# Kernel tuning notes

Measured on AMD Instinct MI355X. Metric: run time of the kernel, lower is better.

## Reference

```python
import jax, jax.numpy as jnp
import numpy as np

K_NEIGH = 5          # topk(..., k=5) hardcoded in compute_distance
CLIP = 1.0 - 1e-7    # keep arccos/grad finite under fp roundoff of unit-quat dots


def setup_inputs() -> dict:
    key = jax.random.key(0)
    k1, k2 = jax.random.split(key)
    pose = jax.random.normal(k1, (1024, 21, 4), dtype=jnp.float32)
    tp = jax.random.normal(k2, (10000, 21, 4), dtype=jnp.float32)
    # train_poses are unit quaternions per joint (module assumes pre-normalized bank)
    train_poses = tp / jnp.linalg.norm(tp, axis=-1, keepdims=True)
    return {"pose": pose, "train_poses": train_poses}


def reference(pose, train_poses):
    # F.normalize(pose, dim=2): unit quaternion per joint
    rand = pose / jnp.linalg.norm(pose, axis=-1, keepdims=True)
    # per-joint quaternion dot: [N, M, 21] (avoids the repeat() materialization of the original)
    dots = jnp.einsum('njd,mjd->nmj', rand, train_poses)
    dots = jnp.clip(dots, -CLIP, CLIP)
    # geodesic distance: sum_j arccos(dot_j) / 2  -> [N, M]
    dist = jnp.sum(jnp.arccos(dots), axis=2) * 0.5
    # smallest-5 neighbors along M, then mean -> [N]
    neg_top, _ = jax.lax.top_k(-dist, K_NEIGH)
    dist_vals = jnp.mean(-neg_top, axis=1)
    return dist_vals
```

## Files before the change

### kernel.cpp

```cpp
#include <hip/hip_runtime.h>
#include <math.h>

#define N_POSE   1024
#define M_TRAIN  10000
#define NJOINT   21
#define KNEIGH   5
#define CLIPV    (1.0f - 1e-7f)
#define PI_F     3.14159265358979f
#define HPI_F    1.57079632679490f
#define BIGF     1e30f
#define QN_FLOATS (N_POSE * NJOINT * 4)

__global__ __launch_bounds__(256)
void pose_norm_kernel(const float* __restrict__ pose, float* __restrict__ qn) {
    int i = blockIdx.x * blockDim.x + threadIdx.x;
    if (i >= N_POSE * NJOINT) return;
    float4 v = ((const float4*)pose)[i];
    float inv = rsqrtf(v.x * v.x + v.y * v.y + v.z * v.z + v.w * v.w);
    v.x *= inv; v.y *= inv; v.z *= inv; v.w *= inv;
    ((float4*)qn)[i] = v;
}

__global__ __launch_bounds__(64)
void pose_dist_kernel(const float* __restrict__ qn,
                      const float* __restrict__ train,
                      float* __restrict__ topk,
                      int chunks, int mchunk) {
    const int nb = blockIdx.x / chunks;
    const int cb = blockIdx.x % chunks;
    const int n  = nb * 64 + threadIdx.x;

    float4 q[NJOINT];
    const float4* __restrict__ qp = (const float4*)qn + (size_t)n * NJOINT;
#pragma unroll
    for (int j = 0; j < NJOINT; ++j) q[j] = qp[j];
#pragma unroll
    for (int j = 0; j < NJOINT; ++j)
        asm volatile("" : "+v"(q[j].x), "+v"(q[j].y), "+v"(q[j].z), "+v"(q[j].w));

    float t0 = BIGF, t1 = BIGF, t2 = BIGF, t3 = BIGF, t4 = BIGF;
    const float4* __restrict__ tq = (const float4*)train + (size_t)cb * mchunk * NJOINT;

#pragma unroll 1
    for (int mi = 0; mi < mchunk; ++mi) {
        const float4* __restrict__ tm = tq + (size_t)mi * NJOINT;
        float a0 = 0.f, a1 = 0.f;
#pragma unroll
        for (int j = 0; j < NJOINT; ++j) {
            float4 p = q[j];
            float4 u = tm[j];
            float d = u.x * p.x + u.y * p.y + u.z * p.z + u.w * p.w;
            float a = fminf(fabsf(d), CLIPV);
            float pl = fmaf(a, -0.0187293f, 0.0742610f);
            pl = fmaf(a, pl, -0.2121144f);
            pl = fmaf(a, pl, 1.5707288f);
            float r  = __builtin_amdgcn_sqrtf(1.0f - a) * pl;
            float cs = __builtin_copysignf(HPI_F - r, d);
            if (j & 1) a1 += cs; else a0 += cs;
        }
        float v = (NJOINT * HPI_F - (a0 + a1)) * 0.5f;
        t4 = fminf(t4, fmaxf(t3, v));
        t3 = fminf(t3, fmaxf(t2, v));
        t2 = fminf(t2, fmaxf(t1, v));
        t1 = fminf(t1, fmaxf(t0, v));
        t0 = fminf(t0, v);
    }

    float* w = topk + ((size_t)n * chunks + cb) * KNEIGH;
    w[0] = t0; w[1] = t1; w[2] = t2; w[3] = t3; w[4] = t4;
}

__global__ __launch_bounds__(64)
void pose_reduce_kernel(const float* __restrict__ topk, float* __restrict__ out,
                        int chunks) {
    const int n = blockIdx.x;
    const int lane = threadIdx.x;
    const int total = chunks * KNEIGH;
    const float* __restrict__ w = topk + (size_t)n * total;

    float t0 = BIGF, t1 = BIGF, t2 = BIGF, t3 = BIGF, t4 = BIGF;
    for (int i = lane; i < total; i += 64) {
        float v = w[i];
        t4 = fminf(t4, fmaxf(t3, v));
        t3 = fminf(t3, fmaxf(t2, v));
        t2 = fminf(t2, fmaxf(t1, v));
        t1 = fminf(t1, fmaxf(t0, v));
        t0 = fminf(t0, v);
    }

    float sum = 0.f;
#pragma unroll
    for (int r = 0; r < KNEIGH; ++r) {
        float v = t0; int who = lane;
        for (int off = 32; off; off >>= 1) {
            float ov = __shfl_xor(v, off);
            int   ow = __shfl_xor(who, off);
            if (ov < v || (ov == v && ow < who)) { v = ov; who = ow; }
        }
        sum += v;
        if (lane == who) { t0 = t1; t1 = t2; t2 = t3; t3 = t4; t4 = BIGF; }
    }
    if (lane == 0) out[n] = sum * (1.0f / KNEIGH);
}

extern "C" void kernel_launch(void* const* d_in, const int* in_sizes, int n_in,
                              void* d_out, int out_size, void* d_ws, size_t ws_size,
                              hipStream_t stream) {
    const float* pose  = (const float*)d_in[0];
    const float* train = (const float*)d_in[1];
    float* out  = (float*)d_out;
    float* qn   = (float*)d_ws;
    float* topk = (float*)d_ws + QN_FLOATS;

    size_t base = (size_t)QN_FLOATS * sizeof(float);
    int chunks = 250;
    if (base + (size_t)N_POSE * chunks * KNEIGH * sizeof(float) > ws_size) chunks = 125;
    if (base + (size_t)N_POSE * chunks * KNEIGH * sizeof(float) > ws_size) chunks = 50;
    if (base + (size_t)N_POSE * chunks * KNEIGH * sizeof(float) > ws_size) chunks = 10;
    const int mchunk = M_TRAIN / chunks;

    pose_norm_kernel<<<dim3((N_POSE * NJOINT + 255) / 256), dim3(256), 0, stream>>>(pose, qn);

    dim3 grid1((N_POSE / 64) * chunks);
    pose_dist_kernel<<<grid1, dim3(64), 0, stream>>>(qn, train, topk, chunks, mchunk);

    pose_reduce_kernel<<<dim3(N_POSE), dim3(64), 0, stream>>>(topk, out, chunks);
}
```

Baseline: 107.0 us.

## Split joints across wave halves and combine partial distances with a cross-lane shuffle

Each 64-lane block now covers 32 poses. The two half-waves each handle about half of the 21 joints: 11 for one half, 10 plus a padded zeroed slot for the other. Partial arccos sums are combined with a shuffle across lane 32 before the top-5 update. This halves per-thread register use for query quaternions and doubles the number of blocks, aiming at better occupancy and latency hiding. In exchange it spends one wasted joint slot and a cross-lane shuffle per train sample, and duplicates the top-5 maintenance in both halves.

Result: slower. 155.0 us (+44.9%).

```diff
diff --git a/kernel.cpp b/kernel.cpp
--- a/kernel.cpp
+++ b/kernel.cpp
@@ -6,9 +6,9 @@
 #define NJOINT   21
 #define KNEIGH   5
 #define CLIPV    (1.0f - 1e-7f)
-#define PI_F     3.14159265358979f
 #define HPI_F    1.57079632679490f
 #define BIGF     1e30f
+#define JH       11
 #define QN_FLOATS (N_POSE * NJOINT * 4)
 
 __global__ __launch_bounds__(256)
@@ -26,29 +26,37 @@
                       const float* __restrict__ train,
                       float* __restrict__ topk,
                       int chunks, int mchunk) {
-    const int nb = blockIdx.x / chunks;
-    const int cb = blockIdx.x % chunks;
-    const int n  = nb * 64 + threadIdx.x;
+    const int nb   = blockIdx.x / chunks;
+    const int cb   = blockIdx.x % chunks;
+    const int lane = threadIdx.x;
+    const int h    = lane >> 5;
+    const int n    = nb * 32 + (lane & 31);
+    const int jbase = h * JH;
 
-    float4 q[NJOINT];
-    const float4* __restrict__ qp = (const float4*)qn + (size_t)n * NJOINT;
+    float4 q[JH];
+    const float4* __restrict__ qp = (const float4*)qn + (size_t)n * NJOINT + jbase;
 #pragma unroll
-    for (int j = 0; j < NJOINT; ++j) q[j] = qp[j];
+    for (int jj = 0; jj < JH; ++jj) {
+        int o = jj; if (jbase + jj > NJOINT - 1) o = jj - 1;
+        q[jj] = qp[o];
+    }
 #pragma unroll
-    for (int j = 0; j < NJOINT; ++j)
-        asm volatile("" : "+v"(q[j].x), "+v"(q[j].y), "+v"(q[j].z), "+v"(q[j].w));
+    for (int jj = 0; jj < JH; ++jj)
+        asm volatile("" : "+v"(q[jj].x), "+v"(q[jj].y), "+v"(q[jj].z), "+v"(q[jj].w));
 
     float t0 = BIGF, t1 = BIGF, t2 = BIGF, t3 = BIGF, t4 = BIGF;
-    const float4* __restrict__ tq = (const float4*)train + (size_t)cb * mchunk * NJOINT;
+    const float4* __restrict__ tq =
+        (const float4*)train + (size_t)cb * mchunk * NJOINT + jbase;
 
 #pragma unroll 1
     for (int mi = 0; mi < mchunk; ++mi) {
         const float4* __restrict__ tm = tq + (size_t)mi * NJOINT;
         float a0 = 0.f, a1 = 0.f;
 #pragma unroll
-        for (int j = 0; j < NJOINT; ++j) {
-            float4 p = q[j];
-            float4 u = tm[j];
+        for (int jj = 0; jj < JH; ++jj) {
+            int o = jj; if (jbase + jj > NJOINT - 1) o = jj - 1;
+            float4 p = q[jj];
+            float4 u = tm[o];
             float d = u.x * p.x + u.y * p.y + u.z * p.z + u.w * p.w;
             float a = fminf(fabsf(d), CLIPV);
             float pl = fmaf(a, -0.0187293f, 0.0742610f);
@@ -56,9 +64,11 @@
             pl = fmaf(a, pl, 1.5707288f);
             float r  = __builtin_amdgcn_sqrtf(1.0f - a) * pl;
             float cs = __builtin_copysignf(HPI_F - r, d);
-            if (j & 1) a1 += cs; else a0 += cs;
+            if (jj == JH - 1) cs = h ? 0.f : cs;
+            if (jj & 1) a1 += cs; else a0 += cs;
         }
-        float v = (NJOINT * HPI_F - (a0 + a1)) * 0.5f;
+        float acc = a0 + a1;
+        float v = (NJOINT * HPI_F - (acc + __shfl_xor(acc, 32))) * 0.5f;
         t4 = fminf(t4, fmaxf(t3, v));
         t3 = fminf(t3, fmaxf(t2, v));
         t2 = fminf(t2, fmaxf(t1, v));
@@ -66,8 +76,10 @@
         t0 = fminf(t0, v);
     }
 
-    float* w = topk + ((size_t)n * chunks + cb) * KNEIGH;
-    w[0] = t0; w[1] = t1; w[2] = t2; w[3] = t3; w[4] = t4;
+    if (lane < 32) {
+        float* w = topk + ((size_t)n * chunks + cb) * KNEIGH;
+        w[0] = t0; w[1] = t1; w[2] = t2; w[3] = t3; w[4] = t4;
+    }
 }
 
 __global__ __launch_bounds__(64)
@@ -121,7 +133,7 @@
 
     pose_norm_kernel<<<dim3((N_POSE * NJOINT + 255) / 256), dim3(256), 0, stream>>>(pose, qn);
 
-    dim3 grid1((N_POSE / 64) * chunks);
+    dim3 grid1((N_POSE / 32) * chunks);
     pose_dist_kernel<<<grid1, dim3(64), 0, stream>>>(qn, train, topk, chunks, mchunk);
 
     pose_reduce_kernel<<<dim3(N_POSE), dim3(64), 0, stream>>>(topk, out, chunks);
```

## Split joints across four lanes per pose and reduce partial sums via shuffles

Applied to the files above, without the earlier changes.

Each pose is now handled by four lanes that each take 5 or 6 joints, so a 256-thread block covers 64 poses with four times as many threads and far fewer registers per thread. Partial arccos sums are combined with two xor shuffles. The top-5 is tracked as a max over the sum, with the final distance transform moved into the reduce kernel, and a branch skips the insertion when the value cannot enter the top-5. The cost is redundant top-k work on all lanes, extra shuffles, a masked duplicate joint load for three of the four lane groups, and inline asm loads.

New measurement: 145.6 us. +36.1%, slower.

```diff
diff --git a/kernel.cpp b/kernel.cpp
--- a/kernel.cpp
+++ b/kernel.cpp
@@ -6,10 +6,18 @@
 #define NJOINT   21
 #define KNEIGH   5
 #define CLIPV    (1.0f - 1e-7f)
-#define PI_F     3.14159265358979f
 #define HPI_F    1.57079632679490f
 #define BIGF     1e30f
+#define TPB      256
 #define QN_FLOATS (N_POSE * NJOINT * 4)
+
+typedef float v4f __attribute__((ext_vector_type(4)));
+
+__device__ __forceinline__ v4f qload(const float* a) {
+    v4f r;
+    asm volatile("global_load_dwordx4 %0, %1, off" : "=v"(r) : "v"(a) : "memory");
+    return r;
+}
 
 __global__ __launch_bounds__(256)
 void pose_norm_kernel(const float* __restrict__ pose, float* __restrict__ qn) {
@@ -21,34 +29,41 @@
     ((float4*)qn)[i] = v;
 }
 
-__global__ __launch_bounds__(64)
+__global__ __launch_bounds__(TPB)
 void pose_dist_kernel(const float* __restrict__ qn,
                       const float* __restrict__ train,
                       float* __restrict__ topk,
                       int chunks, int mchunk) {
-    const int nb = blockIdx.x / chunks;
-    const int cb = blockIdx.x % chunks;
-    const int n  = nb * 64 + threadIdx.x;
+    const int nb  = blockIdx.x / chunks;
+    const int cb  = blockIdx.x % chunks;
+    const int tid = threadIdx.x;
+    const int wl  = tid & 63;
+    const int h   = wl >> 4;
+    const int n   = nb * 64 + (tid >> 6) * 16 + (wl & 15);
+    const int jbase = (h == 0) ? 0 : (5 * h + 1);
+    const int cnt   = (h == 0) ? 6 : 5;
+    const int off5  = (cnt - 1) * 4;
+    const float mask5 = (h == 0) ? 1.0f : 0.0f;
 
-    float4 q[NJOINT];
-    const float4* __restrict__ qp = (const float4*)qn + (size_t)n * NJOINT;
+    v4f q[6];
+    const float* qb = qn + (size_t)n * (NJOINT * 4) + jbase * 4;
 #pragma unroll
-    for (int j = 0; j < NJOINT; ++j) q[j] = qp[j];
-#pragma unroll
-    for (int j = 0; j < NJOINT; ++j)
-        asm volatile("" : "+v"(q[j].x), "+v"(q[j].y), "+v"(q[j].z), "+v"(q[j].w));
+    for (int jj = 0; jj < 5; ++jj) q[jj] = qload(qb + jj * 4);
+    q[5] = qload(qb + off5);
+    asm volatile("s_waitcnt vmcnt(0)" ::: "memory");
 
-    float t0 = BIGF, t1 = BIGF, t2 = BIGF, t3 = BIGF, t4 = BIGF;
-    const float4* __restrict__ tq = (const float4*)train + (size_t)cb * mchunk * NJOINT;
+    float t0 = -BIGF, t1 = -BIGF, t2 = -BIGF, t3 = -BIGF, t4 = -BIGF;
+    const float* tb = train + (size_t)cb * mchunk * (NJOINT * 4) + jbase * 4;
 
 #pragma unroll 1
     for (int mi = 0; mi < mchunk; ++mi) {
-        const float4* __restrict__ tm = tq + (size_t)mi * NJOINT;
+        const float* tm = tb + (size_t)mi * (NJOINT * 4);
         float a0 = 0.f, a1 = 0.f;
 #pragma unroll
-        for (int j = 0; j < NJOINT; ++j) {
-            float4 p = q[j];
-            float4 u = tm[j];
+        for (int jj = 0; jj < 6; ++jj) {
+            float4 u = (jj < 5) ? ((const float4*)tm)[jj]
+                                : *(const float4*)(tm + off5);
+            v4f p = q[jj];
             float d = u.x * p.x + u.y * p.y + u.z * p.z + u.w * p.w;
             float a = fminf(fabsf(d), CLIPV);
             float pl = fmaf(a, -0.0187293f, 0.0742610f);
@@ -56,18 +71,25 @@
             pl = fmaf(a, pl, 1.5707288f);
             float r  = __builtin_amdgcn_sqrtf(1.0f - a) * pl;
             float cs = __builtin_copysignf(HPI_F - r, d);
-            if (j & 1) a1 += cs; else a0 += cs;
+            if (jj == 5) cs *= mask5;
+            if (jj & 1) a1 += cs; else a0 += cs;
         }
-        float v = (NJOINT * HPI_F - (a0 + a1)) * 0.5f;
-        t4 = fminf(t4, fmaxf(t3, v));
-        t3 = fminf(t3, fmaxf(t2, v));
-        t2 = fminf(t2, fmaxf(t1, v));
-        t1 = fminf(t1, fmaxf(t0, v));
-        t0 = fminf(t0, v);
+        float S = a0 + a1;
+        S += __shfl_xor(S, 16);
+        S += __shfl_xor(S, 32);
+        if (S > t4) {
+            t4 = fmaxf(t4, fminf(t3, S));
+            t3 = fmaxf(t3, fminf(t2, S));
+            t2 = fmaxf(t2, fminf(t1, S));
+            t1 = fmaxf(t1, fminf(t0, S));
+            t0 = fmaxf(t0, S);
+        }
     }
 
-    float* w = topk + ((size_t)n * chunks + cb) * KNEIGH;
-    w[0] = t0; w[1] = t1; w[2] = t2; w[3] = t3; w[4] = t4;
+    if (wl < 16) {
+        float* w = topk + ((size_t)n * chunks + cb) * KNEIGH;
+        w[0] = t0; w[1] = t1; w[2] = t2; w[3] = t3; w[4] = t4;
+    }
 }
 
 __global__ __launch_bounds__(64)
@@ -80,7 +102,7 @@
 
     float t0 = BIGF, t1 = BIGF, t2 = BIGF, t3 = BIGF, t4 = BIGF;
     for (int i = lane; i < total; i += 64) {
-        float v = w[i];
+        float v = (NJOINT * HPI_F - w[i]) * 0.5f;
         t4 = fminf(t4, fmaxf(t3, v));
         t3 = fminf(t3, fmaxf(t2, v));
         t2 = fminf(t2, fmaxf(t1, v));
@@ -122,7 +144,7 @@
     pose_norm_kernel<<<dim3((N_POSE * NJOINT + 255) / 256), dim3(256), 0, stream>>>(pose, qn);
 
     dim3 grid1((N_POSE / 64) * chunks);
-    pose_dist_kernel<<<grid1, dim3(64), 0, stream>>>(qn, train, topk, chunks, mchunk);
+    pose_dist_kernel<<<grid1, dim3(TPB), 0, stream>>>(qn, train, topk, chunks, mchunk);
 
     pose_reduce_kernel<<<dim3(N_POSE), dim3(64), 0, stream>>>(topk, out, chunks);
 }
```

## Stream transposed query joints and process eight train poses per joint

Applied to the files above, without the earlier changes.

The normalization kernel now writes query quaternions in a joint-major transposed layout. The distance kernel streams one joint at a time from that layout instead of holding all 21 quaternions in registers. Each loop step evaluates 8 train poses per joint with independent accumulators, and blocks grow from 64 to 256 threads. The aim is to cut VGPR pressure and raise ILP and occupancy, at the cost of re-reading query data from cache on every 8-pose block.

Result: slower. 113.1 us (+5.8%).

```diff
diff --git a/kernel.cpp b/kernel.cpp
--- a/kernel.cpp
+++ b/kernel.cpp
@@ -6,64 +6,75 @@
 #define NJOINT   21
 #define KNEIGH   5
 #define CLIPV    (1.0f - 1e-7f)
-#define PI_F     3.14159265358979f
 #define HPI_F    1.57079632679490f
 #define BIGF     1e30f
-#define QN_FLOATS (N_POSE * NJOINT * 4)
+#define TPB      256
+#define MB       8
+#define QT_FLOATS (N_POSE * NJOINT * 4)
 
 __global__ __launch_bounds__(256)
-void pose_norm_kernel(const float* __restrict__ pose, float* __restrict__ qn) {
+void pose_norm_t_kernel(const float* __restrict__ pose, float* __restrict__ qT) {
     int i = blockIdx.x * blockDim.x + threadIdx.x;
     if (i >= N_POSE * NJOINT) return;
+    int n = i / NJOINT, j = i % NJOINT;
     float4 v = ((const float4*)pose)[i];
     float inv = rsqrtf(v.x * v.x + v.y * v.y + v.z * v.z + v.w * v.w);
     v.x *= inv; v.y *= inv; v.z *= inv; v.w *= inv;
-    ((float4*)qn)[i] = v;
+    ((float4*)qT)[(size_t)j * N_POSE + n] = v;
 }
 
-__global__ __launch_bounds__(64)
-void pose_dist_kernel(const float* __restrict__ qn,
+__global__ __launch_bounds__(TPB)
+void pose_dist_kernel(const float* __restrict__ qT,
                       const float* __restrict__ train,
                       float* __restrict__ topk,
                       int chunks, int mchunk) {
     const int nb = blockIdx.x / chunks;
     const int cb = blockIdx.x % chunks;
-    const int n  = nb * 64 + threadIdx.x;
+    const int n  = nb * TPB + threadIdx.x;
 
-    float4 q[NJOINT];
-    const float4* __restrict__ qp = (const float4*)qn + (size_t)n * NJOINT;
-#pragma unroll
-    for (int j = 0; j < NJOINT; ++j) q[j] = qp[j];
-#pragma unroll
-    for (int j = 0; j < NJOINT; ++j)
-        asm volatile("" : "+v"(q[j].x), "+v"(q[j].y), "+v"(q[j].z), "+v"(q[j].w));
+    const char* tb = (const char*)train + (size_t)cb * mchunk * 336;
+    const float4* __restrict__ qbase = (const float4*)qT + n;
 
     float t0 = BIGF, t1 = BIGF, t2 = BIGF, t3 = BIGF, t4 = BIGF;
-    const float4* __restrict__ tq = (const float4*)train + (size_t)cb * mchunk * NJOINT;
 
 #pragma unroll 1
-    for (int mi = 0; mi < mchunk; ++mi) {
-        const float4* __restrict__ tm = tq + (size_t)mi * NJOINT;
-        float a0 = 0.f, a1 = 0.f;
+    for (int mb = 0; mb < mchunk; mb += MB) {
+        const char* tmb = tb + (size_t)mb * 336;
+        float acc0 = 0.f, acc1 = 0.f, acc2 = 0.f, acc3 = 0.f;
+        float acc4 = 0.f, acc5 = 0.f, acc6 = 0.f, acc7 = 0.f;
+
+        float4 qc = qbase[0];
+#pragma unroll 1
+        for (int j = 0; j < NJOINT; ++j) {
+            float4 qnx = qbase[(j + 1 < NJOINT ? j + 1 : 0) * N_POSE];
 #pragma unroll
-        for (int j = 0; j < NJOINT; ++j) {
-            float4 p = q[j];
-            float4 u = tm[j];
-            float d = u.x * p.x + u.y * p.y + u.z * p.z + u.w * p.w;
-            float a = fminf(fabsf(d), CLIPV);
-            float pl = fmaf(a, -0.0187293f, 0.0742610f);
-            pl = fmaf(a, pl, -0.2121144f);
-            pl = fmaf(a, pl, 1.5707288f);
-            float r  = __builtin_amdgcn_sqrtf(1.0f - a) * pl;
-            float cs = __builtin_copysignf(HPI_F - r, d);
-            if (j & 1) a1 += cs; else a0 += cs;
+            for (int mm = 0; mm < MB; ++mm) {
+                float4 u = *(const float4*)(tmb + mm * 336 + j * 16);
+                float d = u.x * qc.x + u.y * qc.y + u.z * qc.z + u.w * qc.w;
+                float a = fminf(fabsf(d), CLIPV);
+                float pl = fmaf(a, -0.0187293f, 0.0742610f);
+                pl = fmaf(a, pl, -0.2121144f);
+                pl = fmaf(a, pl, 1.5707288f);
+                float r  = __builtin_amdgcn_sqrtf(1.0f - a) * pl;
+                float cs = __builtin_copysignf(HPI_F - r, d);
+                if      (mm == 0) acc0 += cs; else if (mm == 1) acc1 += cs;
+                else if (mm == 2) acc2 += cs; else if (mm == 3) acc3 += cs;
+                else if (mm == 4) acc4 += cs; else if (mm == 5) acc5 += cs;
+                else if (mm == 6) acc6 += cs; else               acc7 += cs;
+            }
+            qc = qnx;
         }
-        float v = (NJOINT * HPI_F - (a0 + a1)) * 0.5f;
-        t4 = fminf(t4, fmaxf(t3, v));
-        t3 = fminf(t3, fmaxf(t2, v));
-        t2 = fminf(t2, fmaxf(t1, v));
-        t1 = fminf(t1, fmaxf(t0, v));
-        t0 = fminf(t0, v);
+
+        float accs[MB] = {acc0, acc1, acc2, acc3, acc4, acc5, acc6, acc7};
+#pragma unroll
+        for (int mm = 0; mm < MB; ++mm) {
+            float v = (NJOINT * HPI_F - accs[mm]) * 0.5f;
+            t4 = fminf(t4, fmaxf(t3, v));
+            t3 = fminf(t3, fmaxf(t2, v));
+            t2 = fminf(t2, fmaxf(t1, v));
+            t1 = fminf(t1, fmaxf(t0, v));
+            t0 = fminf(t0, v);
+        }
     }
 
     float* w = topk + ((size_t)n * chunks + cb) * KNEIGH;
@@ -109,20 +120,20 @@
     const float* pose  = (const float*)d_in[0];
     const float* train = (const float*)d_in[1];
     float* out  = (float*)d_out;
-    float* qn   = (float*)d_ws;
-    float* topk = (float*)d_ws + QN_FLOATS;
+    float* qT   = (float*)d_ws;
+    float* topk = (float*)d_ws + QT_FLOATS;
 
-    size_t base = (size_t)QN_FLOATS * sizeof(float);
+    size_t base = (size_t)QT_FLOATS * sizeof(float);
     int chunks = 250;
     if (base + (size_t)N_POSE * chunks * KNEIGH * sizeof(float) > ws_size) chunks = 125;
     if (base + (size_t)N_POSE * chunks * KNEIGH * sizeof(float) > ws_size) chunks = 50;
     if (base + (size_t)N_POSE * chunks * KNEIGH * sizeof(float) > ws_size) chunks = 10;
     const int mchunk = M_TRAIN / chunks;
 
-    pose_norm_kernel<<<dim3((N_POSE * NJOINT + 255) / 256), dim3(256), 0, stream>>>(pose, qn);
+    pose_norm_t_kernel<<<dim3((N_POSE * NJOINT + 255) / 256), dim3(256), 0, stream>>>(pose, qT);
 
-    dim3 grid1((N_POSE / 64) * chunks);
-    pose_dist_kernel<<<grid1, dim3(64), 0, stream>>>(qn, train, topk, chunks, mchunk);
+    dim3 grid1((N_POSE / TPB) * chunks);
+    pose_dist_kernel<<<grid1, dim3(TPB), 0, stream>>>(qT, train, topk, chunks, mchunk);
 
     pose_reduce_kernel<<<dim3(N_POSE), dim3(64), 0, stream>>>(topk, out, chunks);
 }
```
